# Kernel tuning notes

Measured on AMD Instinct MI355X. Metric: run time of the kernel, lower is better.

The kernel has to match this reference:

```python
import jax, jax.numpy as jnp
import numpy as np

NUM_HEADS = 16


def setup_inputs() -> dict:
    key = jax.random.key(0)
    ks = jax.random.split(key, 7)
    B, N, D = 16, 512, 1024
    return {
        "x": jax.random.normal(ks[0], (B, N, D), dtype=jnp.float32),
        "spatial_encoding": jax.random.normal(ks[1], (B, N, N), dtype=jnp.float32),
        "edge_encoding": jax.random.normal(ks[2], (B, N, N), dtype=jnp.float32),
        "Wq": jax.random.normal(ks[3], (D, D), dtype=jnp.float32) * (D ** -0.5),
        "Wk": jax.random.normal(ks[4], (D, D), dtype=jnp.float32) * (D ** -0.5),
        "Wv": jax.random.normal(ks[5], (D, D), dtype=jnp.float32) * (D ** -0.5),
        "Wo": jax.random.normal(ks[6], (D, D), dtype=jnp.float32) * (D ** -0.5),
    }


def reference(x, spatial_encoding, edge_encoding, Wq, Wk, Wv, Wo):
    B, N, D = x.shape
    H = NUM_HEADS
    hd = D // H
    scale = D ** -0.5  # NOTE: source scales by hidden_dim**-0.5, not head_size**-0.5

    def split_heads(t):  # (B,N,D) -> (B,H,N,hd)
        return t.reshape(B, N, H, hd).transpose(0, 2, 1, 3)

    q = split_heads(x @ Wq.T)
    k = split_heads(x @ Wk.T)
    v = split_heads(x @ Wv.T)

    bias = (spatial_encoding + edge_encoding)[:, None]  # (B,1,N,N)
    a = jnp.einsum("bhnd,bhmd->bhnm", q, k) * scale + bias  # (B,H,N,N)

    # rows that are entirely zero (padded) are masked to -inf
    row_nonzero = jnp.any(a != 0, axis=-1, keepdims=True)  # (B,H,N,1)
    a = jnp.where(row_nonzero, a, -jnp.inf)
    p = jax.nn.softmax(a, axis=-1)
    p = jnp.where(jnp.isnan(p), 0.0, p)  # nan_to_num after softmax of all -inf rows

    o = jnp.einsum("bhnm,bhmd->bhnd", p, v)  # (B,H,N,hd)
    o = o.transpose(0, 2, 1, 3).reshape(B, N, D)
    return o @ Wo.T
```

## Files before the change

kernel.cpp:

```cpp
#include <hip/hip_runtime.h>
#include <cstdint>


typedef unsigned short u16;
typedef unsigned int   u32;
typedef __attribute__((ext_vector_type(8))) short bf8;
typedef __attribute__((ext_vector_type(4))) _Float16 h4;
typedef __attribute__((ext_vector_type(4))) float f4;

__device__ __forceinline__ u16 f2bf(float x) {
  u32 u = __float_as_uint(x);
  u += 0x7FFF + ((u >> 16) & 1);
  return (u16)(u >> 16);
}

__device__ __forceinline__ float bf2f(u16 x) {
  return __uint_as_float(((u32)x) << 16);
}

__device__ __forceinline__ u16 f2h(float x) {
  union { _Float16 h; u16 u; } c;
  c.h = (_Float16)x;
  return c.u;
}

__device__ __forceinline__ void gl2lds16(const void* g, void* l) {
  __builtin_amdgcn_global_load_lds(
      (const __attribute__((address_space(1))) u32*)g,
      (__attribute__((address_space(3))) u32*)l, 16, 0, 0);
}


__global__ __launch_bounds__(256) void prep_kernel(
    const float* __restrict__ x, const float* __restrict__ sp,
    const float* __restrict__ ed,
    const float* __restrict__ W0, const float* __restrict__ W1,
    const float* __restrict__ W2, const float* __restrict__ W3,
    uint4* __restrict__ xb,
    uint4* __restrict__ d0, uint4* __restrict__ d1,
    uint4* __restrict__ d2, uint4* __restrict__ d3,
    u16* __restrict__ Bp) {
  const int bid = blockIdx.x;
  const int tid = threadIdx.x;
  if (bid < 6144) {
    const float* src;
    uint4* dst;
    int j;
    if (bid < 4096) {
      src = x; dst = xb; j = bid * 256 + tid;
    } else {
      const int i = (bid - 4096) * 256 + tid;
      const int w = i >> 17;
      j = i & 131071;
      src = (w == 0) ? W0 : (w == 1) ? W1 : (w == 2) ? W2 : W3;
      dst = (w == 0) ? d0 : (w == 1) ? d1 : (w == 2) ? d2 : d3;
    }
    const float4* s = (const float4*)src;
    const float4 a = s[2 * j], c = s[2 * j + 1];
    uint4 o;
    o.x = (u32)f2bf(a.x) | ((u32)f2bf(a.y) << 16);
    o.y = (u32)f2bf(a.z) | ((u32)f2bf(a.w) << 16);
    o.z = (u32)f2bf(c.x) | ((u32)f2bf(c.y) << 16);
    o.w = (u32)f2bf(c.z) | ((u32)f2bf(c.w) << 16);
    dst[j] = o;
  } else {
    const int id = bid - 6144;
    const int jt = id & 7, qt = (id >> 3) & 7, b = id >> 6;
    const int wave = tid >> 6, quad = (tid >> 4) & 3, l16 = tid & 15;
    const int row = (qt << 6) + (wave << 4) + l16;
    union { u16 a[16]; uint4 v[2]; } tmp;
#pragma unroll
    for (int jb = 0; jb < 4; jb++) {
#pragma unroll
      for (int r = 0; r < 4; r++) {
        const int col = (jt << 6) + (jb << 4) + (quad << 2) + r;
        const size_t idx = ((size_t)b << 18) + (size_t)row * 512 + col;
        tmp.a[jb * 4 + r] = f2bf(sp[idx] + ed[idx]);
      }
    }
    uint4* out = (uint4*)Bp + ((((size_t)b * 8 + qt) * 8 + jt) * 256 + tid) * 2;
    out[0] = tmp.v[0];
    out[1] = tmp.v[1];
  }
}


__device__ __forceinline__ void gemm_core(const u16* __restrict__ A,
                                          const u16* __restrict__ Bt,
                                          int m0, int n0,
                                          u16* lA, u16* lB, f4 acc[4][4]) {
  const int tid  = threadIdx.x;
  const int wave = tid >> 6;
  const int lane = tid & 63;
  const int quad = lane >> 4;
  const int l16  = lane & 15;
  const int wm   = (wave >> 1) << 6;
  const int wn   = (wave & 1) << 6;
  const int srow = tid >> 3;
  const int scol = ((tid & 7) ^ (srow & 7)) << 3;
  const int c0   = (quad ^ (l16 & 7)) << 3;

  f4 zero = {0.f, 0.f, 0.f, 0.f};
#pragma unroll
  for (int mi = 0; mi < 4; mi++)
#pragma unroll
    for (int ni = 0; ni < 4; ni++) acc[mi][ni] = zero;

  const u16* Ab = A  + (size_t)(m0 + srow) * 1024 + scol;
  const u16* Bb = Bt + (size_t)(n0 + srow) * 1024 + scol;

  for (int k0 = 0; k0 < 1024; k0 += 64) {
    __syncthreads();
#pragma unroll
    for (int i = 0; i < 4; i++) {
      gl2lds16(Ab + (size_t)(i << 5) * 1024 + k0,
               (char*)lA + (((i << 8) + (wave << 6)) << 4));
      gl2lds16(Bb + (size_t)(i << 5) * 1024 + k0,
               (char*)lB + (((i << 8) + (wave << 6)) << 4));
    }
    __syncthreads();
#pragma unroll
    for (int kk = 0; kk < 64; kk += 32) {
      const int o = c0 ^ kk;
      bf8 af[4], bfr[4];
#pragma unroll
      for (int mi = 0; mi < 4; mi++)
        af[mi] = *(const bf8*)(lA + (wm + (mi << 4) + l16) * 64 + o);
#pragma unroll
      for (int ni = 0; ni < 4; ni++)
        bfr[ni] = *(const bf8*)(lB + (wn + (ni << 4) + l16) * 64 + o);
#pragma unroll
      for (int mi = 0; mi < 4; mi++)
#pragma unroll
        for (int ni = 0; ni < 4; ni++)
          acc[mi][ni] = __builtin_amdgcn_mfma_f32_16x16x32_bf16(
              af[mi], bfr[ni], acc[mi][ni], 0, 0, 0);
    }
  }
}


__global__ __launch_bounds__(256) void qkv_kernel(
    const u16* __restrict__ xb, const u16* __restrict__ wq,
    const u16* __restrict__ wk, const u16* __restrict__ wv,
    u16* __restrict__ Qh, u16* __restrict__ Kh, u16* __restrict__ Vt) {
  __shared__ __align__(16) u16 lA[128 * 64];
  __shared__ __align__(16) u16 lB[128 * 64];
  const int flat = blockIdx.x + (blockIdx.y << 3) + (blockIdx.z << 9);
  const int m_tile = (flat & 7) | (((flat >> 6) & 7) << 3);
  const int n_tile = (flat >> 3) & 7;
  const int proj = flat >> 9;
  const int m0 = m_tile << 7, n0 = n_tile << 7;
  const u16* W = (proj == 0) ? wq : (proj == 1) ? wk : wv;
  f4 acc[4][4];
  gemm_core(xb, W, m0, n0, lA, lB, acc);

  const int tid = threadIdx.x, wave = tid >> 6, lane = tid & 63;
  const int quad = lane >> 4, l16 = lane & 15;
  const int wm = (wave >> 1) << 6, wn = (wave & 1) << 6;

  if (proj == 2) {
#pragma unroll
    for (int mi = 0; mi < 4; mi++) {
      const int gmb = m0 + wm + (mi << 4) + (quad << 2);
      const int b = gmb >> 9, nb = gmb & 511;
#pragma unroll
      for (int ni = 0; ni < 4; ni++) {
        const int gn = n0 + wn + (ni << 4) + l16;
        const int h = gn >> 6, hdi = gn & 63;
        ushort4 pk;
        pk.x = f2h(acc[mi][ni][0]);
        pk.y = f2h(acc[mi][ni][1]);
        pk.z = f2h(acc[mi][ni][2]);
        pk.w = f2h(acc[mi][ni][3]);
        *(ushort4*)(Vt + ((size_t)((b << 4) + h) * 64 + hdi) * 512 + nb) = pk;
      }
    }
  } else {
    u16* dst = (proj == 0) ? Qh : Kh;
#pragma unroll
    for (int mi = 0; mi < 4; mi++) {
#pragma unroll
      for (int r = 0; r < 4; r++) {
        const int gm = m0 + wm + (mi << 4) + (quad << 2) + r;
        const int b = gm >> 9, n = gm & 511;
#pragma unroll
        for (int ni = 0; ni < 4; ni++) {
          const int gn = n0 + wn + (ni << 4) + l16;
          const int h = gn >> 6, hdi = gn & 63;
          dst[((size_t)((b << 4) + h) * 512 + n) * 64 + hdi] = f2bf(acc[mi][ni][r]);
        }
      }
    }
  }
}


__global__ __launch_bounds__(256) void oproj_kernel(const u16* __restrict__ Ob,
                                                    const u16* __restrict__ wo,
                                                    float* __restrict__ out) {
  __shared__ __align__(16) u16 lA[128 * 64];
  __shared__ __align__(16) u16 lB[128 * 64];
  const int flat = blockIdx.x + (blockIdx.y << 3);
  const int m0 = ((flat & 7) | (((flat >> 6) & 7) << 3)) << 7;
  const int n0 = ((flat >> 3) & 7) << 7;
  f4 acc[4][4];
  gemm_core(Ob, wo, m0, n0, lA, lB, acc);

  const int tid = threadIdx.x, wave = tid >> 6, lane = tid & 63;
  const int quad = lane >> 4, l16 = lane & 15;
  const int wm = (wave >> 1) << 6, wn = (wave & 1) << 6;
#pragma unroll
  for (int mi = 0; mi < 4; mi++)
#pragma unroll
    for (int r = 0; r < 4; r++) {
      const int gm = m0 + wm + (mi << 4) + (quad << 2) + r;
#pragma unroll
      for (int ni = 0; ni < 4; ni++) {
        const int gn = n0 + wn + (ni << 4) + l16;
        out[(size_t)gm * 1024 + gn] = acc[mi][ni][r];
      }
    }
}


__global__ __launch_bounds__(256) void attn_kernel(
    const u16* __restrict__ Qh, const u16* __restrict__ Kh,
    const u16* __restrict__ Vt, const u16* __restrict__ Bp,
    u16* __restrict__ Ob) {
  __shared__ __align__(16) u16 sQ[64 * 64];
  __shared__ __align__(16) u16 sK[64 * 64];
  __shared__ __align__(16) u16 sV[64 * 64];
  const int flat = blockIdx.x + (blockIdx.y << 3) + (blockIdx.z << 7);
  const int qt = (flat >> 3) & 7;
  const int h  = (flat >> 6) & 15;
  const int b  = (flat & 7) | (((flat >> 10) & 1) << 3);
  const int q0 = qt << 6;
  const int tid = threadIdx.x, wave = tid >> 6, lane = tid & 63;
  const int quad = lane >> 4, l16 = lane & 15;
  const int c0  = (quad ^ (l16 & 7)) << 3;
  const int swb = (((tid & 7) ^ ((tid >> 3) & 7)) << 4);

  const u16* Qg = Qh + ((size_t)((b << 4) + h) * 512 + q0) * 64;
  const u16* Kg = Kh + (size_t)((b << 4) + h) * 512 * 64;
  const u16* Vg = Vt + (size_t)((b << 4) + h) * 64 * 512;
  const uint4* Bpg = (const uint4*)Bp + (((size_t)b * 8 + qt) * 8 * 256 + tid) * 2;

#pragma unroll
  for (int i = 0; i < 2; i++) {
    const int e = (i << 8) + tid;
    gl2lds16((const char*)Qg + (e >> 3) * 128 + swb,
             (char*)sQ + (((i << 8) + (wave << 6)) << 4));
  }
  __syncthreads();
  const bf8 bq0 = *(const bf8*)(sQ + ((wave << 4) + l16) * 64 + c0);
  const bf8 bq1 = *(const bf8*)(sQ + ((wave << 4) + l16) * 64 + (c0 ^ 32));

  f4 o[4];
  f4 zero = {0.f, 0.f, 0.f, 0.f};
#pragma unroll
  for (int i = 0; i < 4; i++) o[i] = zero;
  float lsum = 0.f;

  for (int j0 = 0; j0 < 512; j0 += 64) {
    const uint4 bc0 = Bpg[(j0 >> 6) * 512];
    const uint4 bc1 = Bpg[(j0 >> 6) * 512 + 1];
    const u32 bw[8] = {bc0.x, bc0.y, bc0.z, bc0.w, bc1.x, bc1.y, bc1.z, bc1.w};

    __syncthreads();
#pragma unroll
    for (int i = 0; i < 2; i++) {
      const int e = (i << 8) + tid;
      gl2lds16((const char*)Kg + (size_t)j0 * 128 + (e >> 3) * 128 + swb,
               (char*)sK + (((i << 8) + (wave << 6)) << 4));
      gl2lds16((const char*)Vg + (size_t)(e >> 3) * 1024 + j0 * 2 + swb,
               (char*)sV + (((i << 8) + (wave << 6)) << 4));
    }
    __syncthreads();

    h4 pf[4];
#pragma unroll
    for (int jb = 0; jb < 4; jb++) {
      bf8 a0 = *(const bf8*)(sK + ((jb << 4) + l16) * 64 + c0);
      bf8 a1 = *(const bf8*)(sK + ((jb << 4) + l16) * 64 + (c0 ^ 32));
      f4 s = zero;
      s = __builtin_amdgcn_mfma_f32_16x16x32_bf16(a0, bq0, s, 0, 0, 0);
      s = __builtin_amdgcn_mfma_f32_16x16x32_bf16(a1, bq1, s, 0, 0, 0);
#pragma unroll
      for (int r = 0; r < 4; r++) {
        const u32 w = bw[jb * 2 + (r >> 1)];
        const float bias = bf2f((r & 1) ? (u16)(w >> 16) : (u16)(w & 0xFFFF));
        const float ev = __expf(s[r] * 0.03125f + bias);
        lsum += ev;
        pf[jb][r] = (_Float16)ev;
      }
    }

#pragma unroll
    for (int db = 0; db < 4; db++) {
#pragma unroll
      for (int jb = 0; jb < 4; jb++) {
        const h4 va = *(const h4*)(sV + ((db << 4) + l16) * 64 +
                                   ((((jb << 1) + (quad >> 1)) ^ (l16 & 7)) << 3) +
                                   ((quad & 1) << 2));
        o[db] = __builtin_amdgcn_mfma_f32_16x16x16f16(va, pf[jb], o[db], 0, 0, 0);
      }
    }
  }

  lsum += __shfl_xor(lsum, 16);
  lsum += __shfl_xor(lsum, 32);
  const float inv = 1.f / lsum;
  const int q = q0 + (wave << 4) + l16;
#pragma unroll
  for (int db = 0; db < 4; db++) {
    ushort4 pk;
    pk.x = f2bf(o[db][0] * inv);
    pk.y = f2bf(o[db][1] * inv);
    pk.z = f2bf(o[db][2] * inv);
    pk.w = f2bf(o[db][3] * inv);
    *(ushort4*)(Ob + (size_t)((b << 9) + q) * 1024 + (h << 6) + (db << 4) +
                (quad << 2)) = pk;
  }
}


extern "C" void kernel_launch(void* const* d_in, const int* in_sizes, int n_in,
                              void* d_out, int out_size, void* d_ws, size_t ws_size,
                              hipStream_t stream) {
  const float* x  = (const float*)d_in[0];
  const float* sp = (const float*)d_in[1];
  const float* ed = (const float*)d_in[2];
  const float* Wq = (const float*)d_in[3];
  const float* Wk = (const float*)d_in[4];
  const float* Wv = (const float*)d_in[5];
  const float* Wo = (const float*)d_in[6];
  float* out = (float*)d_out;

  char* w = (char*)d_ws;
  u16* xb  = (u16*)(w);
  u16* wqb = (u16*)(w + 16777216);
  u16* wkb = (u16*)(w + 18874368);
  u16* wvb = (u16*)(w + 20971520);
  u16* wob = (u16*)(w + 23068672);
  u16* Qh  = (u16*)(w + 25165824);
  u16* Kh  = (u16*)(w + 41943040);
  u16* Vt  = (u16*)(w + 58720256);
  u16* Ob  = (u16*)(w + 75497472);
  u16* Bp  = (u16*)(w + 92274688);

  prep_kernel<<<7168, 256, 0, stream>>>(x, sp, ed, Wq, Wk, Wv, Wo,
                                        (uint4*)xb, (uint4*)wqb, (uint4*)wkb,
                                        (uint4*)wvb, (uint4*)wob, Bp);
  qkv_kernel<<<dim3(8, 64, 3), 256, 0, stream>>>(xb, wqb, wkb, wvb, Qh, Kh, Vt);
  attn_kernel<<<dim3(8, 16, 16), 256, 0, stream>>>(Qh, Kh, Vt, Bp, Ob);
  oproj_kernel<<<dim3(8, 64, 1), 256, 0, stream>>>(Ob, wob, out);
}
```

Before: 252.1 us.

## Double-buffer K/V in attention, coalesce bias prep, retile output projection

The attention kernel now double-buffers K/V tiles in LDS and prefetches the next bias fragment, so global loads for the next tile overlap with the current tile's MFMA work. It also drops one barrier per iteration. The bias prep path now reads sp/ed with coalesced float4 loads and rearranges the data through an LDS tile, replacing strided scalar loads. The output projection switches to 128x64 tiles with an inline loop, doubling the block count for better CU occupancy at the cost of reloading A tiles more often. The attention kernel uses more LDS and relies on the end-of-loop barrier waiting for the async LDS loads.

```diff
diff --git a/kernel.cpp b/kernel.cpp
--- a/kernel.cpp
+++ b/kernel.cpp
@@ -40,6 +40,7 @@
     uint4* __restrict__ d0, uint4* __restrict__ d1,
     uint4* __restrict__ d2, uint4* __restrict__ d3,
     u16* __restrict__ Bp) {
+  __shared__ u16 sB[64 * 66];
   const int bid = blockIdx.x;
   const int tid = threadIdx.x;
   if (bid < 6144) {
@@ -66,18 +67,28 @@
   } else {
     const int id = bid - 6144;
     const int jt = id & 7, qt = (id >> 3) & 7, b = id >> 6;
+    const int lr = tid >> 4;
+    const int lc = (tid & 15) << 2;
+#pragma unroll
+    for (int it = 0; it < 4; it++) {
+      const int row = (it << 4) + lr;
+      const size_t idx = ((size_t)b << 18) +
+                         (size_t)((qt << 6) + row) * 512 + (jt << 6) + lc;
+      const float4 a = *(const float4*)(sp + idx);
+      const float4 c = *(const float4*)(ed + idx);
+      u16* d = sB + row * 66 + lc;
+      d[0] = f2bf(a.x + c.x); d[1] = f2bf(a.y + c.y);
+      d[2] = f2bf(a.z + c.z); d[3] = f2bf(a.w + c.w);
+    }
+    __syncthreads();
     const int wave = tid >> 6, quad = (tid >> 4) & 3, l16 = tid & 15;
-    const int row = (qt << 6) + (wave << 4) + l16;
+    const int row = (wave << 4) + l16;
     union { u16 a[16]; uint4 v[2]; } tmp;
 #pragma unroll
-    for (int jb = 0; jb < 4; jb++) {
-#pragma unroll
-      for (int r = 0; r < 4; r++) {
-        const int col = (jt << 6) + (jb << 4) + (quad << 2) + r;
-        const size_t idx = ((size_t)b << 18) + (size_t)row * 512 + col;
-        tmp.a[jb * 4 + r] = f2bf(sp[idx] + ed[idx]);
-      }
-    }
+    for (int jb = 0; jb < 4; jb++)
+#pragma unroll
+      for (int r = 0; r < 4; r++)
+        tmp.a[jb * 4 + r] = sB[row * 66 + (jb << 4) + (quad << 2) + r];
     uint4* out = (uint4*)Bp + ((((size_t)b * 8 + qt) * 8 + jt) * 256 + tid) * 2;
     out[0] = tmp.v[0];
     out[1] = tmp.v[1];
@@ -200,23 +211,70 @@
                                                     const u16* __restrict__ wo,
                                                     float* __restrict__ out) {
   __shared__ __align__(16) u16 lA[128 * 64];
-  __shared__ __align__(16) u16 lB[128 * 64];
+  __shared__ __align__(16) u16 lB[64 * 64];
   const int flat = blockIdx.x + (blockIdx.y << 3);
-  const int m0 = ((flat & 7) | (((flat >> 6) & 7) << 3)) << 7;
-  const int n0 = ((flat >> 3) & 7) << 7;
-  f4 acc[4][4];
-  gemm_core(Ob, wo, m0, n0, lA, lB, acc);
-
-  const int tid = threadIdx.x, wave = tid >> 6, lane = tid & 63;
-  const int quad = lane >> 4, l16 = lane & 15;
-  const int wm = (wave >> 1) << 6, wn = (wave & 1) << 6;
+  const int m_tile = (flat & 7) | (((flat >> 7) & 7) << 3);
+  const int n_tile = (flat >> 3) & 15;
+  const int m0 = m_tile << 7, n0 = n_tile << 6;
+
+  const int tid  = threadIdx.x;
+  const int wave = tid >> 6;
+  const int lane = tid & 63;
+  const int quad = lane >> 4;
+  const int l16  = lane & 15;
+  const int wm   = (wave >> 1) << 6;
+  const int wn   = (wave & 1) << 5;
+  const int srow = tid >> 3;
+  const int scol = ((tid & 7) ^ (srow & 7)) << 3;
+  const int c0   = (quad ^ (l16 & 7)) << 3;
+
+  f4 zero = {0.f, 0.f, 0.f, 0.f};
+  f4 acc[4][2];
+#pragma unroll
+  for (int mi = 0; mi < 4; mi++)
+#pragma unroll
+    for (int ni = 0; ni < 2; ni++) acc[mi][ni] = zero;
+
+  const u16* Ab = Ob + (size_t)(m0 + srow) * 1024 + scol;
+  const u16* Bb = wo + (size_t)(n0 + srow) * 1024 + scol;
+
+  for (int k0 = 0; k0 < 1024; k0 += 64) {
+    __syncthreads();
+#pragma unroll
+    for (int i = 0; i < 4; i++)
+      gl2lds16(Ab + (size_t)(i << 5) * 1024 + k0,
+               (char*)lA + (((i << 8) + (wave << 6)) << 4));
+#pragma unroll
+    for (int i = 0; i < 2; i++)
+      gl2lds16(Bb + (size_t)(i << 5) * 1024 + k0,
+               (char*)lB + (((i << 8) + (wave << 6)) << 4));
+    __syncthreads();
+#pragma unroll
+    for (int kk = 0; kk < 64; kk += 32) {
+      const int o = c0 ^ kk;
+      bf8 af[4], bfr[2];
+#pragma unroll
+      for (int mi = 0; mi < 4; mi++)
+        af[mi] = *(const bf8*)(lA + (wm + (mi << 4) + l16) * 64 + o);
+#pragma unroll
+      for (int ni = 0; ni < 2; ni++)
+        bfr[ni] = *(const bf8*)(lB + (wn + (ni << 4) + l16) * 64 + o);
+#pragma unroll
+      for (int mi = 0; mi < 4; mi++)
+#pragma unroll
+        for (int ni = 0; ni < 2; ni++)
+          acc[mi][ni] = __builtin_amdgcn_mfma_f32_16x16x32_bf16(
+              af[mi], bfr[ni], acc[mi][ni], 0, 0, 0);
+    }
+  }
+
 #pragma unroll
   for (int mi = 0; mi < 4; mi++)
 #pragma unroll
     for (int r = 0; r < 4; r++) {
       const int gm = m0 + wm + (mi << 4) + (quad << 2) + r;
 #pragma unroll
-      for (int ni = 0; ni < 4; ni++) {
+      for (int ni = 0; ni < 2; ni++) {
         const int gn = n0 + wn + (ni << 4) + l16;
         out[(size_t)gm * 1024 + gn] = acc[mi][ni][r];
       }
@@ -229,8 +287,8 @@
     const u16* __restrict__ Vt, const u16* __restrict__ Bp,
     u16* __restrict__ Ob) {
   __shared__ __align__(16) u16 sQ[64 * 64];
-  __shared__ __align__(16) u16 sK[64 * 64];
-  __shared__ __align__(16) u16 sV[64 * 64];
+  __shared__ __align__(16) u16 sK[2][64 * 64];
+  __shared__ __align__(16) u16 sV[2][64 * 64];
   const int flat = blockIdx.x + (blockIdx.y << 3) + (blockIdx.z << 7);
   const int qt = (flat >> 3) & 7;
   const int h  = (flat >> 6) & 15;
@@ -246,11 +304,14 @@
   const u16* Vg = Vt + (size_t)((b << 4) + h) * 64 * 512;
   const uint4* Bpg = (const uint4*)Bp + (((size_t)b * 8 + qt) * 8 * 256 + tid) * 2;
 
+  const int rowK = ((tid >> 3) & 31) * 128 + swb;
 #pragma unroll
   for (int i = 0; i < 2; i++) {
     const int e = (i << 8) + tid;
-    gl2lds16((const char*)Qg + (e >> 3) * 128 + swb,
-             (char*)sQ + (((i << 8) + (wave << 6)) << 4));
+    const int ldso = ((i << 8) + (wave << 6)) << 4;
+    gl2lds16((const char*)Qg + (e >> 3) * 128 + swb, (char*)sQ + ldso);
+    gl2lds16((const char*)Kg + (e >> 3) * 128 + swb, (char*)sK[0] + ldso);
+    gl2lds16((const char*)Vg + (size_t)(e >> 3) * 1024 + swb, (char*)sV[0] + ldso);
   }
   __syncthreads();
   const bf8 bq0 = *(const bf8*)(sQ + ((wave << 4) + l16) * 64 + c0);
@@ -262,27 +323,35 @@
   for (int i = 0; i < 4; i++) o[i] = zero;
   float lsum = 0.f;
 
+  uint4 nb0 = Bpg[0], nb1 = Bpg[1];
+
   for (int j0 = 0; j0 < 512; j0 += 64) {
-    const uint4 bc0 = Bpg[(j0 >> 6) * 512];
-    const uint4 bc1 = Bpg[(j0 >> 6) * 512 + 1];
+    const int cur = (j0 >> 6) & 1;
+    const uint4 bc0 = nb0, bc1 = nb1;
     const u32 bw[8] = {bc0.x, bc0.y, bc0.z, bc0.w, bc1.x, bc1.y, bc1.z, bc1.w};
 
-    __syncthreads();
-#pragma unroll
-    for (int i = 0; i < 2; i++) {
-      const int e = (i << 8) + tid;
-      gl2lds16((const char*)Kg + (size_t)j0 * 128 + (e >> 3) * 128 + swb,
-               (char*)sK + (((i << 8) + (wave << 6)) << 4));
-      gl2lds16((const char*)Vg + (size_t)(e >> 3) * 1024 + j0 * 2 + swb,
-               (char*)sV + (((i << 8) + (wave << 6)) << 4));
-    }
-    __syncthreads();
-
+    if (j0 < 448) {
+      const int jn = j0 + 64;
+      nb0 = Bpg[(jn >> 6) * 512];
+      nb1 = Bpg[(jn >> 6) * 512 + 1];
+#pragma unroll
+      for (int i = 0; i < 2; i++) {
+        const int e = (i << 8) + tid;
+        const int ldso = ((i << 8) + (wave << 6)) << 4;
+        gl2lds16((const char*)Kg + (size_t)jn * 128 + (e >> 3) * 128 + swb,
+                 (char*)sK[cur ^ 1] + ldso);
+        gl2lds16((const char*)Vg + (size_t)(e >> 3) * 1024 + jn * 2 + swb,
+                 (char*)sV[cur ^ 1] + ldso);
+      }
+    }
+
+    const u16* sKc = sK[cur];
+    const u16* sVc = sV[cur];
     h4 pf[4];
 #pragma unroll
     for (int jb = 0; jb < 4; jb++) {
-      bf8 a0 = *(const bf8*)(sK + ((jb << 4) + l16) * 64 + c0);
-      bf8 a1 = *(const bf8*)(sK + ((jb << 4) + l16) * 64 + (c0 ^ 32));
+      bf8 a0 = *(const bf8*)(sKc + ((jb << 4) + l16) * 64 + c0);
+      bf8 a1 = *(const bf8*)(sKc + ((jb << 4) + l16) * 64 + (c0 ^ 32));
       f4 s = zero;
       s = __builtin_amdgcn_mfma_f32_16x16x32_bf16(a0, bq0, s, 0, 0, 0);
       s = __builtin_amdgcn_mfma_f32_16x16x32_bf16(a1, bq1, s, 0, 0, 0);
@@ -300,12 +369,13 @@
     for (int db = 0; db < 4; db++) {
 #pragma unroll
       for (int jb = 0; jb < 4; jb++) {
-        const h4 va = *(const h4*)(sV + ((db << 4) + l16) * 64 +
+        const h4 va = *(const h4*)(sVc + ((db << 4) + l16) * 64 +
                                    ((((jb << 1) + (quad >> 1)) ^ (l16 & 7)) << 3) +
                                    ((quad & 1) << 2));
         o[db] = __builtin_amdgcn_mfma_f32_16x16x16f16(va, pf[jb], o[db], 0, 0, 0);
       }
     }
+    __syncthreads();
   }
 
   lsum += __shfl_xor(lsum, 16);
@@ -354,5 +424,5 @@
                                         (uint4*)wvb, (uint4*)wob, Bp);
   qkv_kernel<<<dim3(8, 64, 3), 256, 0, stream>>>(xb, wqb, wkb, wvb, Qh, Kh, Vt);
   attn_kernel<<<dim3(8, 16, 16), 256, 0, stream>>>(Qh, Kh, Vt, Bp, Ob);
-  oproj_kernel<<<dim3(8, 64, 1), 256, 0, stream>>>(Ob, wob, out);
-}
+  oproj_kernel<<<dim3(8, 128), 256, 0, stream>>>(Ob, wob, out);
+}
```

Result: slower. 258.7 us (+2.6%).
